# Kernel tuning notes

Hardware: AMD Instinct MI355X
Metric: run time of the kernel (lower is better)

## Reference

```python
import jax, jax.numpy as jnp
import numpy as np

B, T, C, H, TT = 8, 1024, 512, 8, 4  # batch, seq, n_embd, n_head, total_timestep
D = C // H


def setup_inputs() -> dict:
    key = jax.random.key(0)
    ks = jax.random.split(key, 4)
    s = 1.0 / np.sqrt(C)
    return {
        "x": jax.random.normal(ks[0], (B, T, C), jnp.float32),
        "padding_mask": jax.random.bernoulli(ks[1], 0.1, (TT, T)),  # bool
        "W_qkv": jax.random.normal(ks[2], (C, 3 * C), jnp.float32) * s,
        "b_qkv": jnp.zeros((3 * C,), jnp.float32),
        "W_proj": jax.random.normal(ks[3], (C, C), jnp.float32) * s,
        "b_proj": jnp.zeros((C,), jnp.float32),
    }


def reference(x, padding_mask, W_qkv, b_qkv, W_proj, b_proj):
    # fused QKV projection
    qkv = x @ W_qkv + b_qkv                       # [B,T,3C]
    q, k, v = jnp.split(qkv, 3, axis=-1)
    q = q.reshape(B, T, H, D)
    k = k.reshape(B, T, H, D)
    v = v.reshape(B, T, H, D)

    # mask: causal OR padding (True = attend), replicating torch semantics
    causal = jnp.tril(jnp.ones((T, T), bool))                 # [T,T]
    m = causal[None] | padding_mask[:, :, None]               # [TT,T,T]
    mask = jnp.broadcast_to(m[None], (B // TT, TT, T, T)).reshape(B, 1, T, T)

    scores = jnp.einsum("bqhd,bkhd->bhqk", q, k) * (1.0 / np.sqrt(D))
    scores = jnp.where(mask, scores, jnp.float32(-1e30))
    attn = jax.nn.softmax(scores, axis=-1)                    # [B,H,T,T]
    y = jnp.einsum("bhqk,bkhd->bqhd", attn, v).reshape(B, T, C)
    return y @ W_proj + b_proj
```

## Files before the change

kernel.cpp:

```cpp
#include <hip/hip_runtime.h>
#include <hip/hip_bf16.h>

#define BB 8
#define TT_ 4
#define TSEQ 1024
#define CEMB 512
#define NH 8
#define HD 64

typedef __attribute__((ext_vector_type(8))) short bf16x8;
typedef __attribute__((ext_vector_type(4))) float f32x4;
typedef __attribute__((ext_vector_type(16))) float f32x16;

#define AS1 __attribute__((address_space(1)))
#define AS3 __attribute__((address_space(3)))

__device__ __forceinline__ void gload_lds16(const void* g, void* l) {
  __builtin_amdgcn_global_load_lds((const AS1 unsigned int*)g, (AS3 unsigned int*)l, 16, 0, 0);
}

__device__ __forceinline__ short f2b(float f) {
  union { float f; unsigned u; } v; v.f = f;
  unsigned r = v.u + 0x7FFFu + ((v.u >> 16) & 1u);
  return (short)(r >> 16);
}

__device__ __forceinline__ unsigned pack2(float a, float b) {
  unsigned r;
  asm("v_cvt_pk_bf16_f32 %0, %1, %2" : "=v"(r) : "v"(a), "v"(b));
  return r;
}

__global__ __launch_bounds__(256) void k_prep(
    const float* __restrict__ x, short* __restrict__ xb,
    const float* __restrict__ w0, short* __restrict__ t0,
    const float* __restrict__ w1, short* __restrict__ t1)
{
  __shared__ float tsh[64][65];
  const int bid = blockIdx.x;

  if (bid < 2048) {
    const int i = bid * 256 + threadIdx.x;
    float4 v0 = ((const float4*)x)[i * 2];
    float4 v1 = ((const float4*)x)[i * 2 + 1];
    union { unsigned u[4]; bf16x8 v; } o;
    o.u[0] = pack2(v0.x, v0.y); o.u[1] = pack2(v0.z, v0.w);
    o.u[2] = pack2(v1.x, v1.y); o.u[3] = pack2(v1.z, v1.w);
    ((bf16x8*)xb)[i] = o.v;
    return;
  }

  const int z = (bid >= 2240);
  const int tile = z ? (bid - 2240) : (bid - 2048);
  const int ntx = z ? 8 : 24;
  const float* w = z ? w1 : w0;
  short* wt = z ? t1 : t0;
  const int N = z ? 512 : 1536, K = 512;
  const int tx = threadIdx.x & 15, ty = threadIdx.x >> 4;
  const int n0 = (tile % ntx) * 64, k0 = (tile / ntx) * 64;
#pragma unroll
  for (int i = 0; i < 4; ++i) {
    int kr = i * 16 + ty;
    float4 v = *(const float4*)&w[(size_t)(k0 + kr) * N + n0 + tx * 4];
    tsh[tx * 4 + 0][kr] = v.x; tsh[tx * 4 + 1][kr] = v.y;
    tsh[tx * 4 + 2][kr] = v.z; tsh[tx * 4 + 3][kr] = v.w;
  }
  __syncthreads();
#pragma unroll
  for (int i = 0; i < 4; ++i) {
    int nr = i * 16 + ty;
    short4 o;
    o.x = f2b(tsh[nr][tx * 4 + 0]); o.y = f2b(tsh[nr][tx * 4 + 1]);
    o.z = f2b(tsh[nr][tx * 4 + 2]); o.w = f2b(tsh[nr][tx * 4 + 3]);
    *(short4*)&wt[(size_t)(n0 + nr) * K + k0 + tx * 4] = o;
  }
}

__global__ __launch_bounds__(256) void k_gemm0(
    const short* __restrict__ A, const short* __restrict__ Bt,
    const float* __restrict__ bias,
    short* __restrict__ qb, short* __restrict__ kb, short* __restrict__ vtb,
    const void* __restrict__ pin, int* __restrict__ pme,
    int* __restrict__ perm, int* __restrict__ chunk_nkt)
{
  __shared__ short As[3][128 * 32];
  __shared__ short Bs[3][128 * 32];

  if (blockIdx.x == 768) {
    __shared__ int bad_f32, any_f32, bad_i32, any_i32, bad_u16, any_u16;
    if (threadIdx.x == 0) { bad_f32 = any_f32 = bad_i32 = any_i32 = bad_u16 = any_u16 = 0; }
    __syncthreads();
    const unsigned char* pb = (const unsigned char*)pin;
    const float* pf = (const float*)pin;
    const int* pi = (const int*)pin;
    const unsigned short* ph = (const unsigned short*)pin;
    for (int i = threadIdx.x; i < 1024; i += 256) {
      float fv = pf[i];
      if (fv != 0.0f && fv != 1.0f) bad_f32 = 1;
      if (fv == 1.0f) any_f32 = 1;
      int iv = pi[i];
      if (iv != 0 && iv != 1) bad_i32 = 1;
      if (iv == 1) any_i32 = 1;
    }
    for (int i = threadIdx.x; i < 2048; i += 256) {
      unsigned short hv = ph[i];
      if (hv != 0 && hv != 0x3F80u && hv != 0x3C00u) bad_u16 = 1;
      if (hv == 0x3F80u || hv == 0x3C00u) any_u16 = 1;
    }
    __syncthreads();
    int mode = 3;
    if (!bad_f32 && any_f32) mode = 0;
    else if (!bad_i32 && any_i32) mode = 1;
    else if (!bad_u16 && any_u16) mode = 2;
    for (int i = threadIdx.x; i < TT_ * TSEQ; i += 256) {
      int v;
      if (mode == 0)      v = (pf[i] != 0.0f);
      else if (mode == 1) v = (pi[i] != 0);
      else if (mode == 2) v = (ph[i] != 0);
      else                v = (pb[i] != 0);
      pme[i] = v;
    }
    __syncthreads();
    const int w = threadIdx.x >> 6, lane = threadIdx.x & 63;
    {
      const int* rowp = pme + w * 1024;
      unsigned long long bal[16];
      int npm = 0;
#pragma unroll
      for (int g = 0; g < 16; ++g) {
        bal[g] = __ballot(rowp[g * 64 + lane] != 0);
        npm += __popcll(bal[g]);
      }
      int off_non = 0, off_pm = 1024 - npm;
#pragma unroll
      for (int g = 0; g < 16; ++g) {
        unsigned long long m = bal[g];
        int below = __popcll(m & ((1ull << lane) - 1ull));
        int ispm = (int)((m >> lane) & 1ull);
        int pos = ispm ? (off_pm + below) : (off_non + lane - below);
        perm[w * 1024 + pos] = g * 64 + lane;
        int c = __popcll(m);
        off_pm += c; off_non += 64 - c;
      }
    }
    __syncthreads();
    {
      const int tt = w, c = (lane >> 3) & 7, seg = lane & 7;
      int mx = 0;
#pragma unroll
      for (int i = 0; i < 16; ++i) {
        int q = perm[tt * 1024 + c * 128 + seg * 16 + i];
        int need = pme[tt * 1024 + q] ? 16 : ((q >> 6) + 1);
        mx = mx > need ? mx : need;
      }
#pragma unroll
      for (int s = 1; s < 8; s <<= 1) {
        int o = __shfl_xor(mx, s, 64);
        mx = mx > o ? mx : o;
      }
      if (seg == 0) chunk_nkt[tt * 8 + c] = mx;
    }
    return;
  }

  const int tid = threadIdx.x, lane = tid & 63, w = tid >> 6;
  const int wm = w >> 1, wn = w & 1;
  const int idp = (blockIdx.x & 7) * 96 + (blockIdx.x >> 3);
  const int n0 = (idp % 12) * 128, m0 = (idp / 12) * 128;
  f32x4 acc[4][4] = {};
  const char* Abase = (const char*)A + (size_t)m0 * 1024;
  const char* Bbase = (const char*)Bt + (size_t)n0 * 1024;
  const int rowL = w * 16 + (lane >> 2);
  const int colB = (lane & 3) * 16;

  auto stage = [&](int buf, int k0) {
#pragma unroll
    for (int is = 0; is < 2; ++is) {
      int row = is * 64 + rowL;
      gload_lds16(Abase + (size_t)row * 1024 + (size_t)(k0 * 2 + colB),
                  (char*)As[buf] + is * 4096 + w * 1024);
      gload_lds16(Bbase + (size_t)row * 1024 + (size_t)(k0 * 2 + colB),
                  (char*)Bs[buf] + is * 4096 + w * 1024);
    }
  };

  stage(0, 0);
  stage(1, 32);
#pragma unroll
  for (int it = 0; it < 16; ++it) {
    if (it < 15) asm volatile("s_waitcnt vmcnt(4)\n\ts_barrier" ::: "memory");
    else         asm volatile("s_waitcnt vmcnt(0)\n\ts_barrier" ::: "memory");
    if (it + 2 < 16) stage((it + 2) % 3, (it + 2) * 32);
    const short* Ab = As[it % 3];
    const short* Bb = Bs[it % 3];
    bf16x8 a[4], bfr[4];
#pragma unroll
    for (int mf = 0; mf < 4; ++mf)
      a[mf] = *(const bf16x8*)&Ab[(wm * 64 + mf * 16 + (lane & 15)) * 32 + (lane >> 4) * 8];
#pragma unroll
    for (int nf = 0; nf < 4; ++nf)
      bfr[nf] = *(const bf16x8*)&Bb[(wn * 64 + nf * 16 + (lane & 15)) * 32 + (lane >> 4) * 8];
#pragma unroll
    for (int mf = 0; mf < 4; ++mf)
#pragma unroll
      for (int nf = 0; nf < 4; ++nf)
        acc[mf][nf] = __builtin_amdgcn_mfma_f32_16x16x32_bf16(a[mf], bfr[nf], acc[mf][nf], 0, 0, 0);
  }

#pragma unroll
  for (int nf = 0; nf < 4; ++nf) {
    const int n_g = n0 + wn * 64 + nf * 16 + (lane & 15);
    const float bv = bias[n_g];
    const int which = n_g >> 9;
    const int c = n_g & 511;
    const int h = c >> 6, d = c & 63;
    const float qsc = (which == 0) ? 0.18033688011112043f : 1.0f;
#pragma unroll
    for (int mf = 0; mf < 4; ++mf) {
      const int mb = m0 + wm * 64 + mf * 16 + ((lane >> 4) << 2);
      const int b = mb >> 10, t0 = mb & 1023;
      const int b8h = b * NH + h;
      if (which == 2) {
        short4 pk;
        pk.x = f2b(acc[mf][nf][0] + bv);
        pk.y = f2b(acc[mf][nf][1] + bv);
        pk.z = f2b(acc[mf][nf][2] + bv);
        pk.w = f2b(acc[mf][nf][3] + bv);
        *(short4*)&vtb[((size_t)b8h * HD + d) * TSEQ + t0] = pk;
      } else {
        short* dst = (which == 0) ? qb : kb;
        size_t base = ((size_t)b8h * TSEQ + t0) * HD + d;
#pragma unroll
        for (int r = 0; r < 4; ++r)
          dst[base + (size_t)r * HD] = f2b((acc[mf][nf][r] + bv) * qsc);
      }
    }
  }
}

__global__ __launch_bounds__(256) void k_gemm1(
    const short* __restrict__ A, const short* __restrict__ Bt,
    const float* __restrict__ bias, float* __restrict__ fout)
{
  __shared__ short As[3][64 * 32];
  __shared__ short Bs[3][128 * 32];
  const int tid = threadIdx.x, lane = tid & 63, w = tid >> 6;
  const int wm = w >> 1, wn = w & 1;
  const int idp = (blockIdx.x & 7) * 64 + (blockIdx.x >> 3);
  const int n0 = (idp & 3) * 128, m0 = (idp >> 2) * 64;
  f32x4 acc[2][4] = {};
  const char* Abase = (const char*)A + (size_t)m0 * 1024;
  const char* Bbase = (const char*)Bt + (size_t)n0 * 1024;
  const int rowL = tid >> 2;
  const int colB = (tid & 3) * 16;

  auto stage = [&](int buf, int k0) {
    gload_lds16(Abase + (size_t)rowL * 1024 + (size_t)(k0 * 2 + colB),
                (char*)As[buf] + w * 1024);
#pragma unroll
    for (int is = 0; is < 2; ++is) {
      int row = is * 64 + rowL;
      gload_lds16(Bbase + (size_t)row * 1024 + (size_t)(k0 * 2 + colB),
                  (char*)Bs[buf] + is * 4096 + w * 1024);
    }
  };

  stage(0, 0);
  stage(1, 32);
#pragma unroll
  for (int it = 0; it < 16; ++it) {
    if (it < 15) asm volatile("s_waitcnt vmcnt(3)\n\ts_barrier" ::: "memory");
    else         asm volatile("s_waitcnt vmcnt(0)\n\ts_barrier" ::: "memory");
    if (it + 2 < 16) stage((it + 2) % 3, (it + 2) * 32);
    const short* Ab = As[it % 3];
    const short* Bb = Bs[it % 3];
    bf16x8 a[2], bfr[4];
#pragma unroll
    for (int mf = 0; mf < 2; ++mf)
      a[mf] = *(const bf16x8*)&Ab[(wm * 32 + mf * 16 + (lane & 15)) * 32 + (lane >> 4) * 8];
#pragma unroll
    for (int nf = 0; nf < 4; ++nf)
      bfr[nf] = *(const bf16x8*)&Bb[(wn * 64 + nf * 16 + (lane & 15)) * 32 + (lane >> 4) * 8];
#pragma unroll
    for (int mf = 0; mf < 2; ++mf)
#pragma unroll
      for (int nf = 0; nf < 4; ++nf)
        acc[mf][nf] = __builtin_amdgcn_mfma_f32_16x16x32_bf16(a[mf], bfr[nf], acc[mf][nf], 0, 0, 0);
  }

#pragma unroll
  for (int nf = 0; nf < 4; ++nf) {
    const int n_g = n0 + wn * 64 + nf * 16 + (lane & 15);
    const float bv = bias[n_g];
#pragma unroll
    for (int mf = 0; mf < 2; ++mf) {
      const int mb = m0 + wm * 32 + mf * 16 + ((lane >> 4) << 2);
#pragma unroll
      for (int r = 0; r < 4; ++r)
        fout[(size_t)(mb + r) * 512 + n_g] = acc[mf][nf][r] + bv;
    }
  }
}

__device__ __forceinline__ void pv_step(
    f32x16 p, int sub, int hi, int lq, const char* Vsb, f32x16& o0, f32x16& o1)
{
  unsigned P2[8];
#pragma unroll
  for (int i = 0; i < 8; ++i) P2[i] = pack2(p[2 * i], p[2 * i + 1]);
  unsigned e0 = __shfl_xor(hi ? P2[0] : P2[2], 32, 64);
  unsigned e1 = __shfl_xor(hi ? P2[1] : P2[3], 32, 64);
  unsigned e2 = __shfl_xor(hi ? P2[4] : P2[6], 32, 64);
  unsigned e3 = __shfl_xor(hi ? P2[5] : P2[7], 32, 64);
  union { unsigned u[4]; bf16x8 v; } f0, f1;
  f0.u[0] = hi ? e0 : P2[0]; f0.u[1] = hi ? e1 : P2[1];
  f0.u[2] = hi ? P2[2] : e0; f0.u[3] = hi ? P2[3] : e1;
  f1.u[0] = hi ? e2 : P2[4]; f1.u[1] = hi ? e3 : P2[5];
  f1.u[2] = hi ? P2[6] : e2; f1.u[3] = hi ? P2[7] : e3;
  __builtin_amdgcn_s_setprio(1);
#pragma unroll
  for (int dt = 0; dt < 2; ++dt) {
    int row = dt * 32 + lq;
    bf16x8 v0 = *(const bf16x8*)(Vsb + row * 128 + ((4 * sub + hi) ^ (row & 7)) * 16);
    bf16x8 v1 = *(const bf16x8*)(Vsb + row * 128 + ((4 * sub + 2 + hi) ^ (row & 7)) * 16);
    f32x16& o = dt ? o1 : o0;
    o = __builtin_amdgcn_mfma_f32_32x32x16_bf16(v0, f0.v, o, 0, 0, 0);
    o = __builtin_amdgcn_mfma_f32_32x32x16_bf16(v1, f1.v, o, 0, 0, 0);
  }
  __builtin_amdgcn_s_setprio(0);
}

__global__ __launch_bounds__(512) void k_attn(
    const short* __restrict__ qg, const short* __restrict__ kg,
    const short* __restrict__ vtg, const int* __restrict__ pme,
    const int* __restrict__ perm, const int* __restrict__ chunk_nkt,
    short* __restrict__ yb)
{
  __shared__ char smem[65536];
  const int tid = threadIdx.x, lane = tid & 63, w = tid >> 6;
  const int g = w >> 2;
  const int hi = lane >> 5, lq = lane & 31;
  const int id = blockIdx.x;
  const int bh = id & 63, b = bh >> 3, h = bh & 7, tt = b & 3;
  const int p = id >> 6;
  const int chunk = (p < 4) ? (7 - p) : (p - 4);
  const char* Qb = (const char*)(qg + (size_t)bh * TSEQ * HD);
  const char* Kb = (const char*)(kg + (size_t)bh * TSEQ * HD);
  const char* Vb = (const char*)(vtg + (size_t)bh * HD * TSEQ);

  const int stg_row = ((w & 3) << 3) + (lane >> 3);
  const int stg_cl = (lane & 7) ^ ((lane >> 3) & 7);

  auto stage = [&](int buf, int kt) {
#pragma unroll
    for (int is = 0; is < 2; ++is) {
      int row = is * 32 + stg_row;
      gload_lds16(Kb + (size_t)(kt * 64 + row) * 128 + stg_cl * 16,
                  smem + buf * 8192 + is * 4096 + (w & 3) * 1024);
      gload_lds16(Vb + (size_t)row * 2048 + kt * 128 + stg_cl * 16,
                  smem + 32768 + buf * 8192 + is * 4096 + (w & 3) * 1024);
    }
  };

  const int nkt = chunk_nkt[tt * 8 + chunk];
  const int q_g = perm[tt * 1024 + chunk * 128 + (w & 3) * 32 + lq];
  const int pmrow = pme[tt * TSEQ + q_g];

  if (g < nkt) stage(g * 2, g);

  int wmq = q_g, wnq = q_g;
#pragma unroll
  for (int s = 1; s < 64; s <<= 1) {
    wmq = max(wmq, __shfl_xor(wmq, s, 64));
    wnq = min(wnq, __shfl_xor(wnq, s, 64));
  }
  const int whaspm = __any(pmrow != 0);

  bf16x8 qf[4];
#pragma unroll
  for (int dk = 0; dk < 4; ++dk)
    qf[dk] = *(const bf16x8*)(Qb + (size_t)q_g * 128 + dk * 32 + hi * 16);

  float mrun = -1e30f, lrun = 0.0f;
  f32x16 o0 = {}, o1 = {};

  const int niter = (nkt + 1) >> 1;
  for (int i = 0; i < niter; ++i) {
    asm volatile("s_waitcnt vmcnt(0)" ::: "memory");
    __builtin_amdgcn_s_barrier();
    const int kt = 2 * i + g;
    if (kt + 2 < nkt) stage(g * 2 + ((i + 1) & 1), kt + 2);

    const int kb_ = kt * 64;
    if (kt < nkt && (kb_ <= wmq || whaspm)) {
      const char* Ksb = smem + (g * 2 + (i & 1)) * 8192;
      const char* Vsb = smem + 32768 + (g * 2 + (i & 1)) * 8192;

      f32x16 s0 = {}, s1 = {};
      __builtin_amdgcn_s_setprio(1);
#pragma unroll
      for (int dk = 0; dk < 4; ++dk) {
        int row0 = lq, row1 = 32 + lq;
        bf16x8 kf0 = *(const bf16x8*)(Ksb + row0 * 128 + ((2 * dk + hi) ^ (row0 & 7)) * 16);
        bf16x8 kf1 = *(const bf16x8*)(Ksb + row1 * 128 + ((2 * dk + hi) ^ (row1 & 7)) * 16);
        s0 = __builtin_amdgcn_mfma_f32_32x32x16_bf16(kf0, qf[dk], s0, 0, 0, 0);
        s1 = __builtin_amdgcn_mfma_f32_32x32x16_bf16(kf1, qf[dk], s1, 0, 0, 0);
      }
      __builtin_amdgcn_s_setprio(0);

      if (kb_ + 63 <= wnq) {
      } else if (kb_ > wmq) {
#pragma unroll
        for (int r = 0; r < 16; ++r) {
          s0[r] = pmrow ? s0[r] : -1e30f;
          s1[r] = pmrow ? s1[r] : -1e30f;
        }
      } else {
#pragma unroll
        for (int r = 0; r < 16; ++r) {
          int crow = (r & 3) + 8 * (r >> 2) + 4 * hi;
          s0[r] = ((kb_ + crow <= q_g) || pmrow) ? s0[r] : -1e30f;
          s1[r] = ((kb_ + 32 + crow <= q_g) || pmrow) ? s1[r] : -1e30f;
        }
      }

      float tm[16];
#pragma unroll
      for (int r = 0; r < 16; ++r) tm[r] = fmaxf(s0[r], s1[r]);
#pragma unroll
      for (int st = 8; st >= 1; st >>= 1)
#pragma unroll
        for (int r = 0; r < 8; ++r)
          if (r < st) tm[r] = fmaxf(tm[r], tm[r + st]);
      float mx = fmaxf(tm[0], __shfl_xor(tm[0], 32, 64));
      if (!__all(mx <= mrun + 8.0f)) {
        float nm = fmaxf(mrun, mx);
        float sc = __builtin_amdgcn_exp2f(mrun - nm);
        lrun *= sc;
#pragma unroll
        for (int r = 0; r < 16; ++r) { o0[r] *= sc; o1[r] *= sc; }
        mrun = nm;
      }
#pragma unroll
      for (int r = 0; r < 16; ++r) s0[r] = __builtin_amdgcn_exp2f(s0[r] - mrun);
#pragma unroll
      for (int r = 0; r < 16; ++r) s1[r] = __builtin_amdgcn_exp2f(s1[r] - mrun);
      float ts[16];
#pragma unroll
      for (int r = 0; r < 16; ++r) ts[r] = s0[r] + s1[r];
#pragma unroll
      for (int st = 8; st >= 1; st >>= 1)
#pragma unroll
        for (int r = 0; r < 8; ++r)
          if (r < st) ts[r] = ts[r] + ts[r + st];
      lrun += ts[0] + __shfl_xor(ts[0], 32, 64);

      pv_step(s0, 0, hi, lq, Vsb, o0, o1);
      pv_step(s1, 1, hi, lq, Vsb, o0, o1);
    }
  }

  __syncthreads();
  float* mg = (float*)smem;
  const int idx = (w & 3) * 64 + lane;
  if (g == 1) {
    mg[idx * 34 + 0] = mrun;
    mg[idx * 34 + 1] = lrun;
#pragma unroll
    for (int j = 0; j < 16; ++j) mg[idx * 34 + 2 + j] = o0[j];
#pragma unroll
    for (int j = 0; j < 16; ++j) mg[idx * 34 + 18 + j] = o1[j];
  }
  __syncthreads();
  if (g == 0) {
    const float mB = mg[idx * 34 + 0], lB = mg[idx * 34 + 1];
    const float m = fmaxf(mrun, mB);
    const float wa = __builtin_amdgcn_exp2f(mrun - m);
    const float wb = __builtin_amdgcn_exp2f(mB - m);
    const float linv = 1.0f / (lrun * wa + lB * wb);
    const float fa = wa * linv, fb = wb * linv;
    short* yrow = yb + ((size_t)b * TSEQ + q_g) * CEMB + h * HD;
#pragma unroll
    for (int dt = 0; dt < 2; ++dt) {
      const f32x16& o = dt ? o1 : o0;
      const int ob = dt ? 18 : 2;
#pragma unroll
      for (int gg = 0; gg < 4; ++gg) {
        short4 pk;
        pk.x = f2b(o[4 * gg + 0] * fa + mg[idx * 34 + ob + 4 * gg + 0] * fb);
        pk.y = f2b(o[4 * gg + 1] * fa + mg[idx * 34 + ob + 4 * gg + 1] * fb);
        pk.z = f2b(o[4 * gg + 2] * fa + mg[idx * 34 + ob + 4 * gg + 2] * fb);
        pk.w = f2b(o[4 * gg + 3] * fa + mg[idx * 34 + ob + 4 * gg + 3] * fb);
        *(short4*)(yrow + dt * 32 + 8 * gg + 4 * hi) = pk;
      }
    }
  }
}

extern "C" void kernel_launch(void* const* d_in, const int* in_sizes, int n_in,
                              void* d_out, int out_size, void* d_ws, size_t ws_size,
                              hipStream_t stream) {
  const float* x     = (const float*)d_in[0];
  const void*  pmask = d_in[1];
  const float* Wqkv  = (const float*)d_in[2];
  const float* bqkv  = (const float*)d_in[3];
  const float* Wproj = (const float*)d_in[4];
  const float* bproj = (const float*)d_in[5];
  float* out = (float*)d_out;
  char* ws = (char*)d_ws;

  const size_t OFF_XB   = 0;
  const size_t OFF_WQT  = 8388608;
  const size_t OFF_WPT  = 9961472;
  const size_t OFF_Q    = 10485760;
  const size_t OFF_K    = 18874368;
  const size_t OFF_VT   = 27262976;
  const size_t OFF_Y    = 35651584;
  const size_t OFF_PM   = 44040192;
  const size_t OFF_PERM = 44056576;
  const size_t OFF_CNKT = 44072960;
  const size_t NEED     = 44073984;
  if (ws_size < NEED) return;

  short* xb  = (short*)(ws + OFF_XB);
  short* wqT = (short*)(ws + OFF_WQT);
  short* wpT = (short*)(ws + OFF_WPT);
  short* qb  = (short*)(ws + OFF_Q);
  short* kb  = (short*)(ws + OFF_K);
  short* vtb = (short*)(ws + OFF_VT);
  short* yb  = (short*)(ws + OFF_Y);
  int*   pme = (int*)(ws + OFF_PM);
  int*   prm = (int*)(ws + OFF_PERM);
  int*   cnk = (int*)(ws + OFF_CNKT);

  k_prep<<<dim3(2304), dim3(256), 0, stream>>>(x, xb, Wqkv, wqT, Wproj, wpT);
  k_gemm0<<<dim3(769), dim3(256), 0, stream>>>(xb, wqT, bqkv, qb, kb, vtb,
                                               pmask, pme, prm, cnk);
  k_attn<<<dim3(512), dim3(512), 0, stream>>>(qb, kb, vtb, pme, prm, cnk, yb);
  k_gemm1<<<dim3(512), dim3(256), 0, stream>>>(yb, wpT, bproj, out);
}
```

Before: 85.79 us.

## Stage V-transpose epilogue through LDS and move mask prep into prep kernel

The V-projection epilogue now writes tiles into shared memory, which is reused from the GEMM staging buffers, and then emits coalesced 16-byte rows of the transposed V. Before, each lane did scattered short4 stores. The padding-mask decoding, permutation and chunk-count block moves from the QKV GEMM launch into the prep kernel, so the GEMM grid holds only uniform tiles. The cost is an extra pair of barriers in the V blocks, and one more block in the prep kernel.

```diff
diff --git a/kernel.cpp b/kernel.cpp
--- a/kernel.cpp
+++ b/kernel.cpp
@@ -34,7 +34,9 @@
 __global__ __launch_bounds__(256) void k_prep(
     const float* __restrict__ x, short* __restrict__ xb,
     const float* __restrict__ w0, short* __restrict__ t0,
-    const float* __restrict__ w1, short* __restrict__ t1)
+    const float* __restrict__ w1, short* __restrict__ t1,
+    const void* __restrict__ pin, int* __restrict__ pme,
+    int* __restrict__ perm, int* __restrict__ chunk_nkt)
 {
   __shared__ float tsh[64][65];
   const int bid = blockIdx.x;
@@ -50,119 +52,116 @@
     return;
   }
 
-  const int z = (bid >= 2240);
-  const int tile = z ? (bid - 2240) : (bid - 2048);
-  const int ntx = z ? 8 : 24;
-  const float* w = z ? w1 : w0;
-  short* wt = z ? t1 : t0;
-  const int N = z ? 512 : 1536, K = 512;
-  const int tx = threadIdx.x & 15, ty = threadIdx.x >> 4;
-  const int n0 = (tile % ntx) * 64, k0 = (tile / ntx) * 64;
-#pragma unroll
-  for (int i = 0; i < 4; ++i) {
-    int kr = i * 16 + ty;
-    float4 v = *(const float4*)&w[(size_t)(k0 + kr) * N + n0 + tx * 4];
-    tsh[tx * 4 + 0][kr] = v.x; tsh[tx * 4 + 1][kr] = v.y;
-    tsh[tx * 4 + 2][kr] = v.z; tsh[tx * 4 + 3][kr] = v.w;
-  }
+  if (bid < 2304) {
+    const int z = (bid >= 2240);
+    const int tile = z ? (bid - 2240) : (bid - 2048);
+    const int ntx = z ? 8 : 24;
+    const float* w = z ? w1 : w0;
+    short* wt = z ? t1 : t0;
+    const int N = z ? 512 : 1536, K = 512;
+    const int tx = threadIdx.x & 15, ty = threadIdx.x >> 4;
+    const int n0 = (tile % ntx) * 64, k0 = (tile / ntx) * 64;
+#pragma unroll
+    for (int i = 0; i < 4; ++i) {
+      int kr = i * 16 + ty;
+      float4 v = *(const float4*)&w[(size_t)(k0 + kr) * N + n0 + tx * 4];
+      tsh[tx * 4 + 0][kr] = v.x; tsh[tx * 4 + 1][kr] = v.y;
+      tsh[tx * 4 + 2][kr] = v.z; tsh[tx * 4 + 3][kr] = v.w;
+    }
+    __syncthreads();
+#pragma unroll
+    for (int i = 0; i < 4; ++i) {
+      int nr = i * 16 + ty;
+      short4 o;
+      o.x = f2b(tsh[nr][tx * 4 + 0]); o.y = f2b(tsh[nr][tx * 4 + 1]);
+      o.z = f2b(tsh[nr][tx * 4 + 2]); o.w = f2b(tsh[nr][tx * 4 + 3]);
+      *(short4*)&wt[(size_t)(n0 + nr) * K + k0 + tx * 4] = o;
+    }
+    return;
+  }
+
+  __shared__ int bad_f32, any_f32, bad_i32, any_i32, bad_u16, any_u16;
+  if (threadIdx.x == 0) { bad_f32 = any_f32 = bad_i32 = any_i32 = bad_u16 = any_u16 = 0; }
   __syncthreads();
-#pragma unroll
-  for (int i = 0; i < 4; ++i) {
-    int nr = i * 16 + ty;
-    short4 o;
-    o.x = f2b(tsh[nr][tx * 4 + 0]); o.y = f2b(tsh[nr][tx * 4 + 1]);
-    o.z = f2b(tsh[nr][tx * 4 + 2]); o.w = f2b(tsh[nr][tx * 4 + 3]);
-    *(short4*)&wt[(size_t)(n0 + nr) * K + k0 + tx * 4] = o;
+  const unsigned char* pb = (const unsigned char*)pin;
+  const float* pf = (const float*)pin;
+  const int* pi = (const int*)pin;
+  const unsigned short* ph = (const unsigned short*)pin;
+  for (int i = threadIdx.x; i < 1024; i += 256) {
+    float fv = pf[i];
+    if (fv != 0.0f && fv != 1.0f) bad_f32 = 1;
+    if (fv == 1.0f) any_f32 = 1;
+    int iv = pi[i];
+    if (iv != 0 && iv != 1) bad_i32 = 1;
+    if (iv == 1) any_i32 = 1;
+  }
+  for (int i = threadIdx.x; i < 2048; i += 256) {
+    unsigned short hv = ph[i];
+    if (hv != 0 && hv != 0x3F80u && hv != 0x3C00u) bad_u16 = 1;
+    if (hv == 0x3F80u || hv == 0x3C00u) any_u16 = 1;
+  }
+  __syncthreads();
+  int mode = 3;
+  if (!bad_f32 && any_f32) mode = 0;
+  else if (!bad_i32 && any_i32) mode = 1;
+  else if (!bad_u16 && any_u16) mode = 2;
+  for (int i = threadIdx.x; i < TT_ * TSEQ; i += 256) {
+    int v;
+    if (mode == 0)      v = (pf[i] != 0.0f);
+    else if (mode == 1) v = (pi[i] != 0);
+    else if (mode == 2) v = (ph[i] != 0);
+    else                v = (pb[i] != 0);
+    pme[i] = v;
+  }
+  __syncthreads();
+
+  const int w = threadIdx.x >> 6, lane = threadIdx.x & 63;
+  {
+    const int* rowp = pme + w * 1024;
+    unsigned long long bal[16];
+    int npm = 0;
+#pragma unroll
+    for (int g = 0; g < 16; ++g) {
+      bal[g] = __ballot(rowp[g * 64 + lane] != 0);
+      npm += __popcll(bal[g]);
+    }
+    int off_non = 0, off_pm = 1024 - npm;
+#pragma unroll
+    for (int g = 0; g < 16; ++g) {
+      unsigned long long m = bal[g];
+      int below = __popcll(m & ((1ull << lane) - 1ull));
+      int ispm = (int)((m >> lane) & 1ull);
+      int pos = ispm ? (off_pm + below) : (off_non + lane - below);
+      perm[w * 1024 + pos] = g * 64 + lane;
+      int c = __popcll(m);
+      off_pm += c; off_non += 64 - c;
+    }
+  }
+  __syncthreads();
+  {
+    const int tt = w, c = (lane >> 3) & 7, seg = lane & 7;
+    int mx = 0;
+#pragma unroll
+    for (int i = 0; i < 16; ++i) {
+      int q = perm[tt * 1024 + c * 128 + seg * 16 + i];
+      int need = pme[tt * 1024 + q] ? 16 : ((q >> 6) + 1);
+      mx = mx > need ? mx : need;
+    }
+#pragma unroll
+    for (int s = 1; s < 8; s <<= 1) {
+      int o = __shfl_xor(mx, s, 64);
+      mx = mx > o ? mx : o;
+    }
+    if (seg == 0) chunk_nkt[tt * 8 + c] = mx;
   }
 }
 
 __global__ __launch_bounds__(256) void k_gemm0(
     const short* __restrict__ A, const short* __restrict__ Bt,
     const float* __restrict__ bias,
-    short* __restrict__ qb, short* __restrict__ kb, short* __restrict__ vtb,
-    const void* __restrict__ pin, int* __restrict__ pme,
-    int* __restrict__ perm, int* __restrict__ chunk_nkt)
+    short* __restrict__ qb, short* __restrict__ kb, short* __restrict__ vtb)
 {
-  __shared__ short As[3][128 * 32];
-  __shared__ short Bs[3][128 * 32];
-
-  if (blockIdx.x == 768) {
-    __shared__ int bad_f32, any_f32, bad_i32, any_i32, bad_u16, any_u16;
-    if (threadIdx.x == 0) { bad_f32 = any_f32 = bad_i32 = any_i32 = bad_u16 = any_u16 = 0; }
-    __syncthreads();
-    const unsigned char* pb = (const unsigned char*)pin;
-    const float* pf = (const float*)pin;
-    const int* pi = (const int*)pin;
-    const unsigned short* ph = (const unsigned short*)pin;
-    for (int i = threadIdx.x; i < 1024; i += 256) {
-      float fv = pf[i];
-      if (fv != 0.0f && fv != 1.0f) bad_f32 = 1;
-      if (fv == 1.0f) any_f32 = 1;
-      int iv = pi[i];
-      if (iv != 0 && iv != 1) bad_i32 = 1;
-      if (iv == 1) any_i32 = 1;
-    }
-    for (int i = threadIdx.x; i < 2048; i += 256) {
-      unsigned short hv = ph[i];
-      if (hv != 0 && hv != 0x3F80u && hv != 0x3C00u) bad_u16 = 1;
-      if (hv == 0x3F80u || hv == 0x3C00u) any_u16 = 1;
-    }
-    __syncthreads();
-    int mode = 3;
-    if (!bad_f32 && any_f32) mode = 0;
-    else if (!bad_i32 && any_i32) mode = 1;
-    else if (!bad_u16 && any_u16) mode = 2;
-    for (int i = threadIdx.x; i < TT_ * TSEQ; i += 256) {
-      int v;
-      if (mode == 0)      v = (pf[i] != 0.0f);
-      else if (mode == 1) v = (pi[i] != 0);
-      else if (mode == 2) v = (ph[i] != 0);
-      else                v = (pb[i] != 0);
-      pme[i] = v;
-    }
-    __syncthreads();
-    const int w = threadIdx.x >> 6, lane = threadIdx.x & 63;
-    {
-      const int* rowp = pme + w * 1024;
-      unsigned long long bal[16];
-      int npm = 0;
-#pragma unroll
-      for (int g = 0; g < 16; ++g) {
-        bal[g] = __ballot(rowp[g * 64 + lane] != 0);
-        npm += __popcll(bal[g]);
-      }
-      int off_non = 0, off_pm = 1024 - npm;
-#pragma unroll
-      for (int g = 0; g < 16; ++g) {
-        unsigned long long m = bal[g];
-        int below = __popcll(m & ((1ull << lane) - 1ull));
-        int ispm = (int)((m >> lane) & 1ull);
-        int pos = ispm ? (off_pm + below) : (off_non + lane - below);
-        perm[w * 1024 + pos] = g * 64 + lane;
-        int c = __popcll(m);
-        off_pm += c; off_non += 64 - c;
-      }
-    }
-    __syncthreads();
-    {
-      const int tt = w, c = (lane >> 3) & 7, seg = lane & 7;
-      int mx = 0;
-#pragma unroll
-      for (int i = 0; i < 16; ++i) {
-        int q = perm[tt * 1024 + c * 128 + seg * 16 + i];
-        int need = pme[tt * 1024 + q] ? 16 : ((q >> 6) + 1);
-        mx = mx > need ? mx : need;
-      }
-#pragma unroll
-      for (int s = 1; s < 8; s <<= 1) {
-        int o = __shfl_xor(mx, s, 64);
-        mx = mx > o ? mx : o;
-      }
-      if (seg == 0) chunk_nkt[tt * 8 + c] = mx;
-    }
-    return;
-  }
-
+  __shared__ short SM[24576];
   const int tid = threadIdx.x, lane = tid & 63, w = tid >> 6;
   const int wm = w >> 1, wn = w & 1;
   const int idp = (blockIdx.x & 7) * 96 + (blockIdx.x >> 3);
@@ -173,14 +172,17 @@
   const int rowL = w * 16 + (lane >> 2);
   const int colB = (lane & 3) * 16;
 
+  auto Abuf = [&](int buf) -> short* { return SM + buf * 4096; };
+  auto Bbuf = [&](int buf) -> short* { return SM + 12288 + buf * 4096; };
+
   auto stage = [&](int buf, int k0) {
 #pragma unroll
     for (int is = 0; is < 2; ++is) {
       int row = is * 64 + rowL;
       gload_lds16(Abase + (size_t)row * 1024 + (size_t)(k0 * 2 + colB),
-                  (char*)As[buf] + is * 4096 + w * 1024);
+                  (char*)Abuf(buf) + is * 4096 + w * 1024);
       gload_lds16(Bbase + (size_t)row * 1024 + (size_t)(k0 * 2 + colB),
-                  (char*)Bs[buf] + is * 4096 + w * 1024);
+                  (char*)Bbuf(buf) + is * 4096 + w * 1024);
     }
   };
 
@@ -191,8 +193,8 @@
     if (it < 15) asm volatile("s_waitcnt vmcnt(4)\n\ts_barrier" ::: "memory");
     else         asm volatile("s_waitcnt vmcnt(0)\n\ts_barrier" ::: "memory");
     if (it + 2 < 16) stage((it + 2) % 3, (it + 2) * 32);
-    const short* Ab = As[it % 3];
-    const short* Bb = Bs[it % 3];
+    const short* Ab = Abuf(it % 3);
+    const short* Bb = Bbuf(it % 3);
     bf16x8 a[4], bfr[4];
 #pragma unroll
     for (int mf = 0; mf < 4; ++mf)
@@ -207,32 +209,46 @@
         acc[mf][nf] = __builtin_amdgcn_mfma_f32_16x16x32_bf16(a[mf], bfr[nf], acc[mf][nf], 0, 0, 0);
   }
 
-#pragma unroll
-  for (int nf = 0; nf < 4; ++nf) {
-    const int n_g = n0 + wn * 64 + nf * 16 + (lane & 15);
-    const float bv = bias[n_g];
-    const int which = n_g >> 9;
-    const int c = n_g & 511;
-    const int h = c >> 6, d = c & 63;
+  const int which = n0 >> 9;
+  const int b = m0 >> 10, t0 = m0 & 1023;
+  if (which == 2) {
+    __syncthreads();
+#pragma unroll
+    for (int nf = 0; nf < 4; ++nf) {
+      const int cl = wn * 64 + nf * 16 + (lane & 15);
+      const float bv = bias[n0 + cl];
+#pragma unroll
+      for (int mf = 0; mf < 4; ++mf) {
+        const int tl = wm * 64 + mf * 16 + ((lane >> 4) << 2);
+#pragma unroll
+        for (int r = 0; r < 4; ++r)
+          SM[cl * 136 + tl + r] = f2b(acc[mf][nf][r] + bv);
+      }
+    }
+    __syncthreads();
+    const int row = tid >> 1, half = (tid & 1) * 64;
+    const int cg = (n0 & 511) + row;
+    const int h = cg >> 6, d = cg & 63;
+    short* dst = vtb + ((size_t)(b * NH + h) * HD + d) * TSEQ + t0 + half;
+#pragma unroll
+    for (int j = 0; j < 8; ++j)
+      *(bf16x8*)(dst + j * 8) = *(const bf16x8*)&SM[row * 136 + half + j * 8];
+  } else {
     const float qsc = (which == 0) ? 0.18033688011112043f : 1.0f;
-#pragma unroll
-    for (int mf = 0; mf < 4; ++mf) {
-      const int mb = m0 + wm * 64 + mf * 16 + ((lane >> 4) << 2);
-      const int b = mb >> 10, t0 = mb & 1023;
-      const int b8h = b * NH + h;
-      if (which == 2) {
-        short4 pk;
-        pk.x = f2b(acc[mf][nf][0] + bv);
-        pk.y = f2b(acc[mf][nf][1] + bv);
-        pk.z = f2b(acc[mf][nf][2] + bv);
-        pk.w = f2b(acc[mf][nf][3] + bv);
-        *(short4*)&vtb[((size_t)b8h * HD + d) * TSEQ + t0] = pk;
-      } else {
-        short* dst = (which == 0) ? qb : kb;
-        size_t base = ((size_t)b8h * TSEQ + t0) * HD + d;
+    short* dstb = (which == 0) ? qb : kb;
+#pragma unroll
+    for (int nf = 0; nf < 4; ++nf) {
+      const int n_g = n0 + wn * 64 + nf * 16 + (lane & 15);
+      const float bv = bias[n_g];
+      const int c = n_g & 511;
+      const int h = c >> 6, d = c & 63;
+#pragma unroll
+      for (int mf = 0; mf < 4; ++mf) {
+        const int tl = t0 + wm * 64 + mf * 16 + ((lane >> 4) << 2);
+        size_t base = ((size_t)(b * NH + h) * TSEQ + tl) * HD + d;
 #pragma unroll
         for (int r = 0; r < 4; ++r)
-          dst[base + (size_t)r * HD] = f2b((acc[mf][nf][r] + bv) * qsc);
+          dstb[base + (size_t)r * HD] = f2b((acc[mf][nf][r] + bv) * qsc);
       }
     }
   }
@@ -533,9 +549,9 @@
   int*   prm = (int*)(ws + OFF_PERM);
   int*   cnk = (int*)(ws + OFF_CNKT);
 
-  k_prep<<<dim3(2304), dim3(256), 0, stream>>>(x, xb, Wqkv, wqT, Wproj, wpT);
-  k_gemm0<<<dim3(769), dim3(256), 0, stream>>>(xb, wqT, bqkv, qb, kb, vtb,
+  k_prep<<<dim3(2305), dim3(256), 0, stream>>>(x, xb, Wqkv, wqT, Wproj, wpT,
                                                pmask, pme, prm, cnk);
+  k_gemm0<<<dim3(768), dim3(256), 0, stream>>>(xb, wqT, bqkv, qb, kb, vtb);
   k_attn<<<dim3(512), dim3(512), 0, stream>>>(qb, kb, vtb, pme, prm, cnk, yb);
   k_gemm1<<<dim3(512), dim3(256), 0, stream>>>(yb, wpT, bproj, out);
 }
```

After: 87.24 us. Within noise of the previous version (+1.7%).
